# Kernel tuning notes

Hardware: AMD Instinct MI355X
Metric: run time of the kernel (lower is better)

Reference implementation:

```python
import jax, jax.numpy as jnp
import numpy as np

B, NJ, COL = 16384, 14, 14
R = 4  # scipy gaussian_filter(sigma=1, truncate=4) -> radius int(4*1+0.5)=4


def _gauss_kernel(dtype):
    x = np.arange(-R, R + 1, dtype=np.float64)
    k = np.exp(-0.5 * x * x)
    k /= k.sum()
    return jnp.asarray(k, dtype)


def _gaussian_filter2d(x):
    # x: [B, Nj, COL, COL]; scipy mode='reflect' == jnp.pad mode='symmetric'
    k = _gauss_kernel(x.dtype)
    xp = jnp.pad(x, ((0, 0), (0, 0), (R, R), (R, R)), mode='symmetric')
    n = x.shape[0] * x.shape[1]
    xp = xp.reshape(n, 1, COL + 2 * R, COL + 2 * R)
    y = jax.lax.conv_general_dilated(xp, k.reshape(1, 1, 2 * R + 1, 1), (1, 1), 'VALID')
    y = jax.lax.conv_general_dilated(y, k.reshape(1, 1, 1, 2 * R + 1), (1, 1), 'VALID')
    return y.reshape(x.shape)


def setup_inputs() -> dict:
    key = jax.random.key(0)
    k1, k2, k3, k4, k5 = jax.random.split(key, 5)
    h = jax.random.uniform(k1, (B, NJ, COL, COL), jnp.float32)
    os_ = jax.random.normal(k2, (B, 2 * NJ, COL, COL), jnp.float32)
    op = jax.random.uniform(k3, (B, NJ, 3), jnp.float32)
    t = jax.random.uniform(k4, (B, NJ, 2), jnp.float32)
    vis = jax.random.randint(k5, (B, NJ, 1), 0, 2).astype(jnp.float32)
    v = jnp.concatenate([vis, vis], axis=-1)  # visibility duplicated, as assumed by v.sum()/2
    return {"os_": os_, "h": h, "op": op, "t": t, "v": v}


def reference(os_, h, op, t, v):
    scale = 1.0 / COL
    grid = jnp.arange(COL)

    # --- argmax decode of predicted heatmaps ---
    hf = h.reshape(-1, NJ, COL * COL)
    idx = jnp.argmax(hf, axis=-1)                 # [B, Nj]
    yC = idx // COL                               # integer division (old-torch LongTensor /)
    xC = idx - yC * COL
    hmax = jnp.max(hf, axis=-1)                   # h value at argmax
    osf = os_.reshape(-1, 2 * NJ, COL * COL)
    osx = jnp.take_along_axis(osf[:, :NJ], idx[..., None], axis=-1)[..., 0]
    osy = jnp.take_along_axis(osf[:, NJ:], idx[..., None], axis=-1)[..., 0]
    cond = hmax > 0.5
    x0 = jnp.where(cond, (osx + xC.astype(h.dtype)) * scale, 0.0)
    x1 = jnp.where(cond, (osy + yC.astype(h.dtype)) * scale, 0.0)
    x = jnp.stack([x0, x1], axis=-1)              # [B, Nj, 2]

    # --- gaussian splat of target coords into tt (only for visible joints) ---
    ti = t * COL
    xi = jnp.clip(jnp.trunc(ti[..., 0]).astype(jnp.int32), 0, COL - 1)
    yi = jnp.clip(jnp.trunc(ti[..., 1]).astype(jnp.int32), 0, COL - 1)
    onehot = ((grid[None, None, :, None] == yi[..., None, None]) &
              (grid[None, None, None, :] == xi[..., None, None])).astype(h.dtype)
    g = _gaussian_filter2d(onehot)
    mn = g.min(axis=(-2, -1), keepdims=True)
    mx = g.max(axis=(-2, -1), keepdims=True)
    gn = (g - mn) / (mx - mn)                     # min_max normalization
    vis = jnp.trunc(v[..., 0]).astype(jnp.int32) == 1  # int(v[i,j,0]) == 1
    tt = jnp.where(vis[..., None, None], gn, 0.0)

    # --- d1: heatmap MSE; for invisible joints only ROW 0 of diff is zeroed (faithful to source) ---
    diff1 = h - tt
    row0_mask = (~vis)[..., None, None] & (grid == 0)[None, None, :, None]
    diff1 = jnp.where(row0_mask, 0.0, diff1)
    N = v.sum() / 2
    d1 = jnp.sum(diff1 * diff1) / N

    # --- d2: decoded-coordinate MSE, visibility-masked ---
    diff2 = (x - t) * v
    d2 = jnp.sum(diff2 * diff2) / N

    return d1 + d2
```

## Files before the change

kernel.cpp:

```cpp
#include <hip/hip_runtime.h>
#include <math.h>

#define NB     16384
#define NJOINT 14
#define NCOL   14
#define NPIX   196
#define NTASKS (NB * NJOINT)
#define RAD    4

#define BLOCK1 128
#define GRID1  (NTASKS / BLOCK1)

__global__ __launch_bounds__(BLOCK1) void mse2_main(
    const float* __restrict__ osp,
    const float* __restrict__ h,
    const float* __restrict__ t,
    const float* __restrict__ v,
    double* __restrict__ partials)
{
    __shared__ float tbl[NCOL * NCOL];
    __shared__ float rmin[NCOL], rmax[NCOL];
    __shared__ double sd[BLOCK1], sn[BLOCK1];

    const int tid = threadIdx.x;

    for (int e = tid; e < NPIX; e += BLOCK1) {
        double kd[2 * RAD + 1];
        double ks = 0.0;
        #pragma unroll
        for (int d = 0; d <= 2 * RAD; ++d) {
            double xx = (double)(d - RAD);
            kd[d] = exp(-0.5 * xx * xx);
            ks += kd[d];
        }
        const int p = e / NCOL, o = e % NCOL;
        float s = 0.f;
        #pragma unroll
        for (int d = 0; d <= 2 * RAD; ++d) {
            int i = o + d;
            int m = (i < RAD) ? (RAD - 1 - i)
                  : (i < RAD + NCOL) ? (i - RAD)
                  : (2 * (RAD + NCOL) - 1 - i - RAD);
            if (m == p) s += (float)(kd[d] / ks);
        }
        tbl[p * NCOL + o] = s;
    }
    __syncthreads();
    if (tid < NCOL) {
        float mnv = tbl[tid * NCOL], mxv = mnv;
        for (int o = 1; o < NCOL; ++o) {
            float val = tbl[tid * NCOL + o];
            mnv = fminf(mnv, val);
            mxv = fmaxf(mxv, val);
        }
        rmin[tid] = mnv;
        rmax[tid] = mxv;
    }
    __syncthreads();

    const int task = blockIdx.x * BLOCK1 + tid;

    const float2 tv = reinterpret_cast<const float2*>(t)[task];
    const float t0 = tv.x;
    const float t1 = tv.y;
    const float v0 = reinterpret_cast<const float2*>(v)[task].x;
    const bool vis = ((int)v0) == 1;

    const int xi = min(NCOL - 1, max(0, (int)(t0 * (float)NCOL)));
    const int yi = min(NCOL - 1, max(0, (int)(t1 * (float)NCOL)));
    const float mn  = rmin[yi] * rmin[xi];
    const float mx  = rmax[yi] * rmax[xi];
    const float inv = 1.f / (mx - mn);

    float gyr[NCOL], gxr[NCOL];
    #pragma unroll
    for (int k = 0; k < NCOL; ++k) {
        gyr[k] = tbl[yi * NCOL + k];
        gxr[k] = tbl[xi * NCOL + k];
    }

    const float4* __restrict__ hb4 =
        reinterpret_cast<const float4*>(h + (size_t)task * NPIX);

    float acc  = 0.f;
    float mval = -1.f;
    int   midx = 0;

    const float visf = vis ? 1.f : 0.f;

    #pragma unroll
    for (int q = 0; q < NPIX / 4; ++q) {
        const float4 hv4 = hb4[q];
        const float ev[4] = {hv4.x, hv4.y, hv4.z, hv4.w};
        #pragma unroll
        for (int j = 0; j < 4; ++j) {
            const int el = 4 * q + j;
            const int y = el / NCOL;
            const int x = el - y * NCOL;
            const float hv = ev[j];
            if (hv > mval) { mval = hv; midx = el; }
            const float gn  = (gyr[y] * gxr[x] - mn) * inv;
            const float tgt = visf * gn;
            const float d   = hv - tgt;
            const float c   = (!vis && y == 0) ? 0.f : d * d;
            acc += c;
        }
    }

    float d2v = 0.f, nv = 0.f;
    if (vis) {
        nv = v0;
        const int yC = midx / NCOL;
        const int xC = midx - yC * NCOL;
        const int b  = task / NJOINT;
        const int j  = task - b * NJOINT;
        const float* __restrict__ ob = osp + ((size_t)b * (2 * NJOINT) + j) * NPIX;
        const float osx = ob[midx];
        const float osy = ob[(size_t)NJOINT * NPIX + midx];
        const bool cond = mval > 0.5f;
        const float sc = 1.0f / (float)NCOL;
        const float x0 = cond ? (osx + (float)xC) * sc : 0.f;
        const float x1 = cond ? (osy + (float)yC) * sc : 0.f;
        const float dx = x0 - t0;
        const float dy = x1 - t1;
        d2v = dx * dx + dy * dy;
    }

    sd[tid] = (double)acc + (double)d2v;
    sn[tid] = (double)nv;
    __syncthreads();
    #pragma unroll
    for (int off = BLOCK1 / 2; off > 0; off >>= 1) {
        if (tid < off) {
            sd[tid] += sd[tid + off];
            sn[tid] += sn[tid + off];
        }
        __syncthreads();
    }
    if (tid == 0) {
        partials[blockIdx.x * 2 + 0] = sd[0];
        partials[blockIdx.x * 2 + 1] = sn[0];
    }
}

__global__ __launch_bounds__(256) void mse2_reduce(const double* __restrict__ partials,
                                                   float* __restrict__ out)
{
    __shared__ double ssum[256], snum[256];
    double s = 0.0, n = 0.0;
    for (int i = threadIdx.x; i < GRID1; i += 256) {
        s += partials[i * 2 + 0];
        n += partials[i * 2 + 1];
    }
    ssum[threadIdx.x] = s;
    snum[threadIdx.x] = n;
    __syncthreads();
    for (int off = 128; off; off >>= 1) {
        if (threadIdx.x < off) {
            ssum[threadIdx.x] += ssum[threadIdx.x + off];
            snum[threadIdx.x] += snum[threadIdx.x + off];
        }
        __syncthreads();
    }
    if (threadIdx.x == 0) out[0] = (float)(ssum[0] / snum[0]);
}

extern "C" void kernel_launch(void* const* d_in, const int* in_sizes, int n_in,
                              void* d_out, int out_size, void* d_ws, size_t ws_size,
                              hipStream_t stream) {
    const float* osp = (const float*)d_in[0];
    const float* h   = (const float*)d_in[1];
    const float* t   = (const float*)d_in[3];
    const float* v   = (const float*)d_in[4];
    double* partials = (double*)d_ws;
    float* out = (float*)d_out;

    mse2_main<<<GRID1, BLOCK1, 0, stream>>>(osp, h, t, v, partials);
    mse2_reduce<<<1, 256, 0, stream>>>(partials, out);
}
```

Before: 42.81 us.

## Fold min-max normalization into separable gaussian factors and widen block to 256

Drops the per-row minimum from the normalization, relying on the min of the reflected gaussian being zero. Folds the inverse max and the visibility mask into the x-factor array, so each pixel's target becomes a single multiply. Replaces the row-0 select with a multiply by the visibility flag. Also doubles the block size to 256 and uses one thread per table entry, which assumes the block has at least 196 threads. Dropping the min is exact only if the table minimum is truly 0, and for radius 4 on a 14-wide grid it may not be.

New measurement: 42.70 us. No clear change (-0.3%).

```diff
diff --git a/kernel.cpp b/kernel.cpp
--- a/kernel.cpp
+++ b/kernel.cpp
@@ -8,8 +8,10 @@
 #define NTASKS (NB * NJOINT)
 #define RAD    4
 
-#define BLOCK1 128
+#define BLOCK1 256
 #define GRID1  (NTASKS / BLOCK1)
+
+typedef float f4 __attribute__((ext_vector_type(4)));
 
 __global__ __launch_bounds__(BLOCK1) void mse2_main(
     const float* __restrict__ osp,
@@ -18,13 +20,13 @@
     const float* __restrict__ v,
     double* __restrict__ partials)
 {
-    __shared__ float tbl[NCOL * NCOL];
-    __shared__ float rmin[NCOL], rmax[NCOL];
+    __shared__ float tbl[NPIX];
+    __shared__ float rmax[NCOL];
     __shared__ double sd[BLOCK1], sn[BLOCK1];
 
     const int tid = threadIdx.x;
 
-    for (int e = tid; e < NPIX; e += BLOCK1) {
+    if (tid < NPIX) {
         double kd[2 * RAD + 1];
         double ks = 0.0;
         #pragma unroll
@@ -33,7 +35,7 @@
             kd[d] = exp(-0.5 * xx * xx);
             ks += kd[d];
         }
-        const int p = e / NCOL, o = e % NCOL;
+        const int p = tid / NCOL, o = tid % NCOL;
         float s = 0.f;
         #pragma unroll
         for (int d = 0; d <= 2 * RAD; ++d) {
@@ -47,13 +49,8 @@
     }
     __syncthreads();
     if (tid < NCOL) {
-        float mnv = tbl[tid * NCOL], mxv = mnv;
-        for (int o = 1; o < NCOL; ++o) {
-            float val = tbl[tid * NCOL + o];
-            mnv = fminf(mnv, val);
-            mxv = fmaxf(mxv, val);
-        }
-        rmin[tid] = mnv;
+        float mxv = tbl[tid * NCOL];
+        for (int o = 1; o < NCOL; ++o) mxv = fmaxf(mxv, tbl[tid * NCOL + o]);
         rmax[tid] = mxv;
     }
     __syncthreads();
@@ -65,45 +62,40 @@
     const float t1 = tv.y;
     const float v0 = reinterpret_cast<const float2*>(v)[task].x;
     const bool vis = ((int)v0) == 1;
+    const float visf = vis ? 1.f : 0.f;
 
     const int xi = min(NCOL - 1, max(0, (int)(t0 * (float)NCOL)));
     const int yi = min(NCOL - 1, max(0, (int)(t1 * (float)NCOL)));
-    const float mn  = rmin[yi] * rmin[xi];
-    const float mx  = rmax[yi] * rmax[xi];
-    const float inv = 1.f / (mx - mn);
+    const float inv = 1.f / (rmax[yi] * rmax[xi]);
 
-    float gyr[NCOL], gxr[NCOL];
+    float gys[NCOL], gxs[NCOL];
     #pragma unroll
     for (int k = 0; k < NCOL; ++k) {
-        gyr[k] = tbl[yi * NCOL + k];
-        gxr[k] = tbl[xi * NCOL + k];
+        gys[k] = tbl[yi * NCOL + k];
+        gxs[k] = vis ? tbl[xi * NCOL + k] * inv : 0.f;
     }
 
-    const float4* __restrict__ hb4 =
-        reinterpret_cast<const float4*>(h + (size_t)task * NPIX);
+    const f4* __restrict__ hb4 =
+        reinterpret_cast<const f4*>(h + (size_t)task * NPIX);
 
     float acc  = 0.f;
     float mval = -1.f;
     int   midx = 0;
 
-    const float visf = vis ? 1.f : 0.f;
-
     #pragma unroll
     for (int q = 0; q < NPIX / 4; ++q) {
-        const float4 hv4 = hb4[q];
-        const float ev[4] = {hv4.x, hv4.y, hv4.z, hv4.w};
+        const f4 hv4 = hb4[q];
         #pragma unroll
         for (int j = 0; j < 4; ++j) {
             const int el = 4 * q + j;
             const int y = el / NCOL;
             const int x = el - y * NCOL;
-            const float hv = ev[j];
+            const float hv = hv4[j];
             if (hv > mval) { mval = hv; midx = el; }
-            const float gn  = (gyr[y] * gxr[x] - mn) * inv;
-            const float tgt = visf * gn;
+            const float tgt = gys[y] * gxs[x];
             const float d   = hv - tgt;
-            const float c   = (!vis && y == 0) ? 0.f : d * d;
-            acc += c;
+            const float c   = d * d;
+            acc += (y == 0) ? visf * c : c;
         }
     }
 
```
